# Optimization experiments

Measured on AMD Instinct MI355X. Metric: run time of the kernel, lower is better.

The kernel has to match this reference:

```python
import jax, jax.numpy as jnp
import numpy as np

BS, NQ, NK = 2, 2048, 2048
D_OUT, H, D_K, D_V = 1024, 16, 64, 64


def _xavier(key, shape):
    fan_in, fan_out = shape[1], shape[0]
    lim = float(np.sqrt(6.0 / (fan_in + fan_out)))
    return jax.random.uniform(key, shape, jnp.float32, -lim, lim)


def setup_inputs() -> dict:
    key = jax.random.key(0)
    ks = jax.random.split(key, 9)
    return {
        "queries": jax.random.normal(ks[0], (BS, NQ, D_OUT), jnp.float32),
        "keys": jax.random.normal(ks[1], (BS, NK, D_OUT), jnp.float32),
        "values": jax.random.normal(ks[2], (BS, NK, D_OUT), jnp.float32),
        "mask": jax.random.randint(ks[3], (BS, H, NQ, NK), 0, 2).astype(bool),
        "weights": jax.random.uniform(ks[4], (BS, H, NQ, NK), jnp.float32),
        "Wq": _xavier(ks[5], (H * D_K, D_OUT)),
        "bq": jnp.zeros((H * D_K,), jnp.float32),
        "Wk": _xavier(ks[6], (H * D_K, D_OUT)),
        "bk": jnp.zeros((H * D_K,), jnp.float32),
        "Wv": _xavier(ks[7], (H * D_V, D_OUT)),
        "bv": jnp.zeros((H * D_V,), jnp.float32),
        "Wo": _xavier(ks[8], (D_OUT, H * D_V)),
        "bo": jnp.zeros((D_OUT,), jnp.float32),
    }


def reference(queries, keys, values, mask, weights, Wq, bq, Wk, bk, Wv, bv, Wo, bo):
    bs, nq, _ = queries.shape
    nk = keys.shape[1]
    # projections: (bs, n, h*d) -> (bs, h, n, d)
    q = (queries @ Wq.T + bq).reshape(bs, nq, H, D_K).transpose(0, 2, 1, 3)
    k = (keys @ Wk.T + bk).reshape(bs, nk, H, D_K).transpose(0, 2, 1, 3)
    v = (values @ Wv.T + bv).reshape(bs, nk, H, D_V).transpose(0, 2, 1, 3)
    # scaled dot-product scores: (bs, h, nq, nk)
    att = jnp.einsum("bhqd,bhkd->bhqk", q, k) / jnp.sqrt(jnp.float32(D_K))
    att = att * weights                      # elementwise weight bias
    att = jnp.where(mask, -jnp.inf, att)     # masked_fill(mask, -inf)
    att = jax.nn.softmax(att, axis=-1)
    # dropout is identity at p=0 / eval
    out = jnp.einsum("bhqk,bhkd->bhqd", att, v)  # (bs, h, nq, d_v)
    out = out.transpose(0, 2, 1, 3).reshape(bs, nq, H * D_V)
    return out @ Wo.T + bo
```

## Files before the change

kernel.cpp:

```cpp
#include <hip/hip_runtime.h>
#include <stdint.h>

#define DEV __device__ __forceinline__

typedef __attribute__((__ext_vector_type__(8))) short short8;
typedef __attribute__((__ext_vector_type__(4))) short short4_t;
typedef __attribute__((__ext_vector_type__(4))) float f32x4;
typedef __attribute__((__ext_vector_type__(4))) unsigned short ushort4_t;
typedef __attribute__((__ext_vector_type__(4))) _Float16 half4;

#define MFMA16F16(a, b, c) __builtin_amdgcn_mfma_f32_16x16x16f16((a), (b), (c), 0, 0, 0)

DEV unsigned short f2bf(float f) {
  union { float f; unsigned u; } x; x.f = f;
  unsigned u = x.u;
  unsigned r = (u + 0x7FFFu + ((u >> 16) & 1u)) >> 16;
  return (unsigned short)r;
}

DEV unsigned short f2h(float f) {
  _Float16 h = (_Float16)f;
  unsigned short u;
  __builtin_memcpy(&u, &h, 2);
  return u;
}

DEV void gload_lds16(const void* g, void* l) {
  __builtin_amdgcn_global_load_lds(
      (const __attribute__((address_space(1))) unsigned int*)g,
      (__attribute__((address_space(3))) unsigned int*)l,
      16, 0, 0);
}

DEV short8 ld_g8(const unsigned short* p) { return *(const short8*)p; }
DEV short8 ld_s8(const unsigned short* p) { return *(const short8*)p; }

__global__ void detect_mask_fmt(const unsigned int* __restrict__ mask, int* __restrict__ flag) {
  if (threadIdx.x == 0 && blockIdx.x == 0) {
    int fmt = 1;
    for (int i = 0; i < 256; ++i) {
      unsigned u = mask[i];
      if (u == 0x3F800000u) { fmt = 2; break; }
      if ((u & 0xFFFFFF00u) != 0u) { fmt = 0; break; }
    }
    *flag = fmt;
  }
}

__global__ void cvt_all(const float* __restrict__ q, const float* __restrict__ k,
                        const float* __restrict__ v,
                        const float* __restrict__ wq, const float* __restrict__ wk,
                        const float* __restrict__ wv, const float* __restrict__ wo,
                        unsigned short* __restrict__ Xq, unsigned short* __restrict__ Xk,
                        unsigned short* __restrict__ Xv, unsigned short* __restrict__ Wqb,
                        unsigned short* __restrict__ Wkb, unsigned short* __restrict__ Wvb,
                        unsigned short* __restrict__ Wob) {
  int i = blockIdx.x * 256 + threadIdx.x;
  const float* src; unsigned short* dst; int off;
  if (i < 1048576)      { src = q;  dst = Xq;  off = i; }
  else if (i < 2097152) { src = k;  dst = Xk;  off = i - 1048576; }
  else if (i < 3145728) { src = v;  dst = Xv;  off = i - 2097152; }
  else if (i < 3407872) { src = wq; dst = Wqb; off = i - 3145728; }
  else if (i < 3670016) { src = wk; dst = Wkb; off = i - 3407872; }
  else if (i < 3932160) { src = wv; dst = Wvb; off = i - 3670016; }
  else                  { src = wo; dst = Wob; off = i - 3932160; }
  float4 vv = ((const float4*)src)[off];
  ushort4_t r;
  r.x = f2bf(vv.x); r.y = f2bf(vv.y); r.z = f2bf(vv.z); r.w = f2bf(vv.w);
  ((ushort4_t*)dst)[off] = r;
}

__global__ __launch_bounds__(256, 2) void proj_gemm(
    const unsigned short* __restrict__ Xq, const unsigned short* __restrict__ Xk,
    const unsigned short* __restrict__ Xv,
    const unsigned short* __restrict__ Wqb, const unsigned short* __restrict__ Wkb,
    const unsigned short* __restrict__ Wvb,
    const float* __restrict__ bq, const float* __restrict__ bk, const float* __restrict__ bv,
    unsigned short* __restrict__ QP, unsigned short* __restrict__ KP,
    unsigned short* __restrict__ VT) {
  const int tid = threadIdx.x;
  const int wid = tid >> 6, lane = tid & 63;
  const int l16 = lane & 15, hi = lane >> 4;
  const int m0 = blockIdx.x * 128;
  const int sel = blockIdx.y >> 3;
  const int n0 = (blockIdx.y & 7) * 128;

  const unsigned short* X; const unsigned short* W; const float* bias; unsigned short* out;
  if (sel == 0)      { X = Xq; W = Wqb; bias = bq; out = QP; }
  else if (sel == 1) { X = Xk; W = Wkb; bias = bk; out = KP; }
  else               { X = Xv; W = Wvb; bias = bv; out = VT; }

  __shared__ unsigned short stage[2 * 128 * 32];

  f32x4 acc[4][4] = {};
  const int wm = (wid >> 1) * 64, wn = (wid & 1) * 64;
  const int aoff = (sel == 2) ? 4096 : 0;
  const int boff = 4096 - aoff;

  for (int kt = 0; kt < 1024; kt += 32) {
#pragma unroll
    for (int t = 0; t < 4; ++t) {
      int g = wid * 4 + t;
      int c = g & 7;
      int row = c * 16 + (lane >> 2);
      int ko = (lane & 3) * 8;
      const unsigned short* src = (g < 8)
          ? (X + (size_t)(m0 + row) * 1024 + kt + ko)
          : (W + (size_t)(n0 + row) * 1024 + kt + ko);
      gload_lds16(src, (unsigned short*)((char*)stage + g * 1024));
    }
    __syncthreads();

    short8 af[4], bfr[4];
#pragma unroll
    for (int i = 0; i < 4; ++i)
      af[i] = ld_s8(&stage[aoff + (wm + i * 16 + l16) * 32 + hi * 8]);
#pragma unroll
    for (int j = 0; j < 4; ++j)
      bfr[j] = ld_s8(&stage[boff + (wn + j * 16 + l16) * 32 + hi * 8]);
#pragma unroll
    for (int i = 0; i < 4; ++i)
#pragma unroll
      for (int j = 0; j < 4; ++j)
        acc[i][j] = __builtin_amdgcn_mfma_f32_16x16x32_bf16(af[i], bfr[j], acc[i][j], 0, 0, 0);
    __syncthreads();
  }

  if (sel != 2) {
#pragma unroll
    for (int j = 0; j < 4; ++j) {
      int feat = n0 + wn + j * 16 + l16;
      float bi = bias[feat];
      int h = feat >> 6, d = feat & 63;
#pragma unroll
      for (int i = 0; i < 4; ++i) {
#pragma unroll
        for (int r = 0; r < 4; ++r) {
          int m = m0 + wm + i * 16 + hi * 4 + r;
          int b = m >> 11, n = m & 2047;
          float v = acc[i][j][r] + bi;
          out[(((size_t)(b * 16 + h)) * 2048 + n) * 64 + d] = f2bf(v);
        }
      }
    }
  } else {
#pragma unroll
    for (int j = 0; j < 4; ++j) {
      int tc0 = m0 + wn + j * 16;
      int b = tc0 >> 11, n = tc0 & 2047;
#pragma unroll
      for (int i = 0; i < 4; ++i) {
#pragma unroll
        for (int r = 0; r < 4; ++r) {
          int feat = n0 + wm + i * 16 + hi * 4 + r;
          int h = feat >> 6, d = feat & 63;
          float v = acc[i][j][r] + bias[feat];
          out[((size_t)(b * 16 + h) * 64 + d) * 2048 + n + l16] = f2h(v);
        }
      }
    }
  }
}

__global__ __launch_bounds__(256, 4) void attn_kernel(
    const unsigned short* __restrict__ Q, const unsigned short* __restrict__ K,
    const unsigned short* __restrict__ VT,
    const float* __restrict__ weights,
    const unsigned char* __restrict__ mask8, const unsigned int* __restrict__ mask32,
    const int* __restrict__ mfmt,
    unsigned short* __restrict__ O) {
  const int bid = blockIdx.x;
  const int r8 = bid & 7, g = bid >> 3;
  const int qt = g & 31, bh = r8 + 8 * (g >> 5);
  const int b = bh >> 4, h = bh & 15;
  const int tid = threadIdx.x, wid = tid >> 6, lane = tid & 63;
  const int l16 = lane & 15, hi = lane >> 4;
  const size_t bh_nd = (size_t)bh * 2048 * 64;
  const size_t bh_nn = (size_t)bh * 2048 * 2048;
  const int q0 = qt * 64;
  const int qloc = wid * 16 + l16;
  const int fmt = *mfmt;
  const bool staged_mask = (fmt == 0);

  short8 qf[2];
  qf[0] = ld_g8(Q + bh_nd + (size_t)(q0 + qloc) * 64 + hi * 8);
  qf[1] = ld_g8(Q + bh_nd + (size_t)(q0 + qloc) * 64 + 32 + hi * 8);

  __shared__ float wlds[2][64 * 32];
  __shared__ unsigned short vlds[2][64 * 32];
  __shared__ unsigned char mlds[2][64 * 32];

  const int wr8 = lane >> 3;
  const int wcu = (lane & 7) ^ wr8;
  const size_t woff0 = (size_t)(q0 + wid * 16 + wr8) * 2048 + 4 * wcu;
  const int vr = (lane >> 2) & 15;
  const int vcu = (lane & 3) ^ (vr & 3);
  const size_t voff = (size_t)(wid * 16 + vr) * 2048 + 8 * vcu;
  const int mr = lane >> 1;
  const int mcu = (lane & 1) ^ (mr & 1);
  const size_t moff = (size_t)(q0 + wid * 32 + mr) * 2048 + 16 * mcu;

  const float* wsrc = weights + bh_nn;
  const unsigned short* vsrc = VT + bh_nd;
  const unsigned char* msrc = mask8 + bh_nn;

#define STAGE(NXT, KT)                                                         \
  {                                                                            \
    gload_lds16(wsrc + woff0 + (KT), &wlds[NXT][wid * 512]);                   \
    gload_lds16(wsrc + woff0 + 8 * 2048 + (KT), &wlds[NXT][wid * 512 + 256]);  \
    gload_lds16(vsrc + voff + (KT), &vlds[NXT][wid * 512]);                    \
    if (staged_mask && wid < 2)                                                \
      gload_lds16(msrc + moff + (KT), &mlds[NXT][wid * 1024]);                 \
  }

  f32x4 o[4] = {};
  float mrow = -1e30f, lrow = 0.f;

  STAGE(0, 0)
  __syncthreads();

  for (int t = 0; t < 64; ++t) {
    const int cur = t & 1;
    const int kt0 = t * 32;

    short8 kf00 = ld_g8(K + bh_nd + (size_t)(kt0 + l16) * 64 + hi * 8);
    short8 kf01 = ld_g8(K + bh_nd + (size_t)(kt0 + l16) * 64 + 32 + hi * 8);
    short8 kf10 = ld_g8(K + bh_nd + (size_t)(kt0 + 16 + l16) * 64 + hi * 8);
    short8 kf11 = ld_g8(K + bh_nd + (size_t)(kt0 + 16 + l16) * 64 + 32 + hi * 8);

    if (t < 63) STAGE(cur ^ 1, kt0 + 32)

    f32x4 s0 = {}, s1 = {};
    s0 = __builtin_amdgcn_mfma_f32_16x16x32_bf16(kf00, qf[0], s0, 0, 0, 0);
    s0 = __builtin_amdgcn_mfma_f32_16x16x32_bf16(kf01, qf[1], s0, 0, 0, 0);
    s1 = __builtin_amdgcn_mfma_f32_16x16x32_bf16(kf10, qf[0], s1, 0, 0, 0);
    s1 = __builtin_amdgcn_mfma_f32_16x16x32_bf16(kf11, qf[1], s1, 0, 0, 0);

    f32x4 w0 = *(const f32x4*)&wlds[cur][qloc * 32 + 4 * ((hi + 0) ^ (l16 & 7))];
    f32x4 w1 = *(const f32x4*)&wlds[cur][qloc * 32 + 4 * ((hi + 4) ^ (l16 & 7))];
    unsigned mv0, mv1;
    if (staged_mask) {
      mv0 = *(const unsigned*)&mlds[cur][qloc * 32 + 16 * (0 ^ (l16 & 1)) + 4 * hi];
      mv1 = *(const unsigned*)&mlds[cur][qloc * 32 + 16 * (1 ^ (l16 & 1)) + 4 * hi];
    } else {
      mv0 = mv1 = 0;
      const size_t mb = bh_nn + (size_t)(q0 + qloc) * 2048 + kt0 + 4 * hi;
#pragma unroll
      for (int r = 0; r < 4; ++r) {
        mv0 |= (mask32[mb + r] ? 0xFFu : 0u) << (8 * r);
        mv1 |= (mask32[mb + 16 + r] ? 0xFFu : 0u) << (8 * r);
      }
    }
#pragma unroll
    for (int r = 0; r < 4; ++r) {
      s0[r] = ((mv0 >> (8 * r)) & 0xFF) ? -INFINITY : s0[r] * 0.125f * w0[r];
      s1[r] = ((mv1 >> (8 * r)) & 0xFF) ? -INFINITY : s1[r] * 0.125f * w1[r];
    }

    float tm = fmaxf(fmaxf(fmaxf(s0[0], s0[1]), fmaxf(s0[2], s0[3])),
                     fmaxf(fmaxf(s1[0], s1[1]), fmaxf(s1[2], s1[3])));
    tm = fmaxf(tm, __shfl_xor(tm, 16));
    tm = fmaxf(tm, __shfl_xor(tm, 32));
    float mnew = fmaxf(mrow, tm);
    float sc = __expf(mrow - mnew);
    mrow = mnew;
    lrow *= sc;
#pragma unroll
    for (int d0 = 0; d0 < 4; ++d0) {
      o[d0][0] *= sc; o[d0][1] *= sc; o[d0][2] *= sc; o[d0][3] *= sc;
    }
#pragma unroll
    for (int r = 0; r < 4; ++r) {
      s0[r] = __expf(s0[r] - mrow);
      s1[r] = __expf(s1[r] - mrow);
    }
    float ps = s0[0] + s0[1] + s0[2] + s0[3] + s1[0] + s1[1] + s1[2] + s1[3];
    ps += __shfl_xor(ps, 16);
    ps += __shfl_xor(ps, 32);
    lrow += ps;

    half4 p0, p1;
    p0[0] = (_Float16)s0[0]; p0[1] = (_Float16)s0[1];
    p0[2] = (_Float16)s0[2]; p0[3] = (_Float16)s0[3];
    p1[0] = (_Float16)s1[0]; p1[1] = (_Float16)s1[1];
    p1[2] = (_Float16)s1[2]; p1[3] = (_Float16)s1[3];

#pragma unroll
    for (int d0 = 0; d0 < 4; ++d0) {
      union { short4_t s; half4 h; } v0, v1;
      v0.s = *(const short4_t*)&vlds[cur][(d0 * 16 + l16) * 32 +
              8 * ((2 * 0 + (hi >> 1)) ^ (l16 & 3)) + 4 * (hi & 1)];
      v1.s = *(const short4_t*)&vlds[cur][(d0 * 16 + l16) * 32 +
              8 * ((2 * 1 + (hi >> 1)) ^ (l16 & 3)) + 4 * (hi & 1)];
      o[d0] = MFMA16F16(v0.h, p0, o[d0]);
      o[d0] = MFMA16F16(v1.h, p1, o[d0]);
    }

    __syncthreads();
  }

  float inv = 1.0f / lrow;
  const size_t obase = (size_t)(b * 2048 + q0 + qloc) * 1024 + h * 64;
#pragma unroll
  for (int d0 = 0; d0 < 4; ++d0) {
    ushort4_t pk;
    pk.x = f2bf(o[d0][0] * inv); pk.y = f2bf(o[d0][1] * inv);
    pk.z = f2bf(o[d0][2] * inv); pk.w = f2bf(o[d0][3] * inv);
    *(ushort4_t*)&O[obase + d0 * 16 + 4 * hi] = pk;
  }
#undef STAGE
}

__global__ __launch_bounds__(256, 2) void out_gemm(
    const unsigned short* __restrict__ A, const unsigned short* __restrict__ W,
    const float* __restrict__ bias, float* __restrict__ Cout) {
  const int tid = threadIdx.x;
  const int wid = tid >> 6, lane = tid & 63;
  const int l16 = lane & 15, hi = lane >> 4;
  const int m0 = blockIdx.x * 128;
  const int n0 = blockIdx.y * 128;

  __shared__ unsigned short stage[2 * 128 * 32];
  f32x4 acc[4][4] = {};
  const int wm = (wid >> 1) * 64, wn = (wid & 1) * 64;

  for (int kt = 0; kt < 1024; kt += 32) {
#pragma unroll
    for (int t = 0; t < 4; ++t) {
      int g = wid * 4 + t;
      int c = g & 7;
      int row = c * 16 + (lane >> 2);
      int ko = (lane & 3) * 8;
      const unsigned short* src = (g < 8)
          ? (A + (size_t)(m0 + row) * 1024 + kt + ko)
          : (W + (size_t)(n0 + row) * 1024 + kt + ko);
      gload_lds16(src, (unsigned short*)((char*)stage + g * 1024));
    }
    __syncthreads();

    short8 af[4], bfr[4];
#pragma unroll
    for (int i = 0; i < 4; ++i)
      af[i] = ld_s8(&stage[(wm + i * 16 + l16) * 32 + hi * 8]);
#pragma unroll
    for (int j = 0; j < 4; ++j)
      bfr[j] = ld_s8(&stage[4096 + (wn + j * 16 + l16) * 32 + hi * 8]);
#pragma unroll
    for (int i = 0; i < 4; ++i)
#pragma unroll
      for (int j = 0; j < 4; ++j)
        acc[i][j] = __builtin_amdgcn_mfma_f32_16x16x32_bf16(af[i], bfr[j], acc[i][j], 0, 0, 0);
    __syncthreads();
  }

#pragma unroll
  for (int j = 0; j < 4; ++j) {
    int feat = n0 + wn + j * 16 + l16;
    float bi = bias[feat];
#pragma unroll
    for (int i = 0; i < 4; ++i) {
#pragma unroll
      for (int r = 0; r < 4; ++r) {
        int m = m0 + wm + i * 16 + hi * 4 + r;
        Cout[(size_t)m * 1024 + feat] = acc[i][j][r] + bi;
      }
    }
  }
}

extern "C" void kernel_launch(void* const* d_in, const int* in_sizes, int n_in,
                              void* d_out, int out_size, void* d_ws, size_t ws_size,
                              hipStream_t stream) {
  const float* queries = (const float*)d_in[0];
  const float* keys    = (const float*)d_in[1];
  const float* values  = (const float*)d_in[2];
  const void*  maskp   = d_in[3];
  const float* weights = (const float*)d_in[4];
  const float* Wq = (const float*)d_in[5];
  const float* bq = (const float*)d_in[6];
  const float* Wk = (const float*)d_in[7];
  const float* bk = (const float*)d_in[8];
  const float* Wv = (const float*)d_in[9];
  const float* bv = (const float*)d_in[10];
  const float* Wo = (const float*)d_in[11];
  const float* bo = (const float*)d_in[12];

  unsigned short* ws = (unsigned short*)d_ws;
  unsigned short* Xq  = ws;
  unsigned short* Xk  = ws + 4194304;
  unsigned short* Xv  = ws + 8388608;
  unsigned short* Wqb = ws + 12582912;
  unsigned short* Wkb = ws + 13631488;
  unsigned short* Wvb = ws + 14680064;
  unsigned short* Wob = ws + 15728640;
  unsigned short* QP  = ws + 16777216;
  unsigned short* KP  = ws + 20971520;
  unsigned short* VPT = ws + 25165824;
  unsigned short* OB  = Xq;
  int* mflag = (int*)(ws + 29360128);

  detect_mask_fmt<<<1, 64, 0, stream>>>((const unsigned int*)maskp, mflag);

  cvt_all<<<16384, 256, 0, stream>>>(queries, keys, values, Wq, Wk, Wv, Wo,
                                     Xq, Xk, Xv, Wqb, Wkb, Wvb, Wob);

  proj_gemm<<<dim3(32, 24), 256, 0, stream>>>(Xq, Xk, Xv, Wqb, Wkb, Wvb,
                                              bq, bk, bv, QP, KP, VPT);
  attn_kernel<<<1024, 256, 0, stream>>>(
      QP, KP, VPT, weights,
      (const unsigned char*)maskp, (const unsigned int*)maskp, mflag, OB);
  out_gemm<<<dim3(32, 8), 256, 0, stream>>>(OB, Wob, bo, (float*)d_out);
}
```

Baseline: 387.2 us.

## Pack mask to bits and switch attention to 32x32 MFMA with 128-row tiles

Adds a pre-pass that packs the boolean/int mask into 32-bit bitmasks laid out per key tile, so the attention loop reads one word per row instead of staging bytes. The attention kernel now uses 32x32x16 MFMA for both QK and PV with 128 query rows per block, halving the block count and the redundant K/V reads per query. It also skips the rescale when no lane's running max grows. The cost is an extra kernel pass over the full mask, lower occupancy (launch bounds 2), and a larger weights LDS buffer.

Measured after the change: 359.2 us (median of 2 runs). -7.2%, faster.

```diff
diff --git a/kernel.cpp b/kernel.cpp
--- a/kernel.cpp
+++ b/kernel.cpp
@@ -4,12 +4,11 @@
 #define DEV __device__ __forceinline__
 
 typedef __attribute__((__ext_vector_type__(8))) short short8;
-typedef __attribute__((__ext_vector_type__(4))) short short4_t;
 typedef __attribute__((__ext_vector_type__(4))) float f32x4;
+typedef __attribute__((__ext_vector_type__(16))) float f32x16;
 typedef __attribute__((__ext_vector_type__(4))) unsigned short ushort4_t;
 typedef __attribute__((__ext_vector_type__(4))) _Float16 half4;
-
-#define MFMA16F16(a, b, c) __builtin_amdgcn_mfma_f32_16x16x16f16((a), (b), (c), 0, 0, 0)
+typedef __attribute__((__ext_vector_type__(8))) _Float16 half8;
 
 DEV unsigned short f2bf(float f) {
   union { float f; unsigned u; } x; x.f = f;
@@ -34,6 +33,9 @@
 
 DEV short8 ld_g8(const unsigned short* p) { return *(const short8*)p; }
 DEV short8 ld_s8(const unsigned short* p) { return *(const short8*)p; }
+DEV half4 ld_h4(const unsigned short* p) {
+  half4 r; __builtin_memcpy(&r, p, 8); return r;
+}
 
 __global__ void detect_mask_fmt(const unsigned int* __restrict__ mask, int* __restrict__ flag) {
   if (threadIdx.x == 0 && blockIdx.x == 0) {
@@ -44,6 +46,58 @@
       if ((u & 0xFFFFFF00u) != 0u) { fmt = 0; break; }
     }
     *flag = fmt;
+  }
+}
+
+__global__ void pack_mask(const unsigned char* __restrict__ m8,
+                          const unsigned int* __restrict__ m32,
+                          const int* __restrict__ mfmt,
+                          unsigned int* __restrict__ pm) {
+  __shared__ unsigned int tile[32 * 65];
+  const int bh = blockIdx.x >> 6;
+  const int q0 = (blockIdx.x & 63) * 32;
+  const int fmt = *mfmt;
+  const int tid = threadIdx.x;
+#pragma unroll
+  for (int rnd = 0; rnd < 8; ++rnd) {
+    int w = tid + rnd * 256;
+    int q = w >> 6, t = w & 63;
+    size_t sb = ((size_t)(bh * 2048 + q0 + q)) * 2048 + t * 32;
+    unsigned bits = 0;
+    if (fmt == 0) {
+      uint4 a = *(const uint4*)(m8 + sb);
+      uint4 bq = *(const uint4*)(m8 + sb + 16);
+      unsigned wa0 = a.x, wa1 = a.y, wa2 = a.z, wa3 = a.w;
+      unsigned wb0 = bq.x, wb1 = bq.y, wb2 = bq.z, wb3 = bq.w;
+#pragma unroll
+      for (int e = 0; e < 4; ++e) {
+        bits |= (((wa0 >> (8 * e)) & 0xFFu) ? 1u : 0u) << (0 + e);
+        bits |= (((wa1 >> (8 * e)) & 0xFFu) ? 1u : 0u) << (4 + e);
+        bits |= (((wa2 >> (8 * e)) & 0xFFu) ? 1u : 0u) << (8 + e);
+        bits |= (((wa3 >> (8 * e)) & 0xFFu) ? 1u : 0u) << (12 + e);
+        bits |= (((wb0 >> (8 * e)) & 0xFFu) ? 1u : 0u) << (16 + e);
+        bits |= (((wb1 >> (8 * e)) & 0xFFu) ? 1u : 0u) << (20 + e);
+        bits |= (((wb2 >> (8 * e)) & 0xFFu) ? 1u : 0u) << (24 + e);
+        bits |= (((wb3 >> (8 * e)) & 0xFFu) ? 1u : 0u) << (28 + e);
+      }
+    } else {
+#pragma unroll
+      for (int c = 0; c < 8; ++c) {
+        uint4 v = *(const uint4*)(m32 + sb + c * 4);
+        bits |= (v.x ? 1u : 0u) << (c * 4);
+        bits |= (v.y ? 1u : 0u) << (c * 4 + 1);
+        bits |= (v.z ? 1u : 0u) << (c * 4 + 2);
+        bits |= (v.w ? 1u : 0u) << (c * 4 + 3);
+      }
+    }
+    tile[q * 65 + t] = bits;
+  }
+  __syncthreads();
+#pragma unroll
+  for (int rnd = 0; rnd < 8; ++rnd) {
+    int w = tid + rnd * 256;
+    int t = w >> 5, q = w & 31;
+    pm[((size_t)bh * 64 + t) * 2048 + q0 + q] = tile[q * 65 + t];
   }
 }
 
@@ -162,58 +216,47 @@
   }
 }
 
-__global__ __launch_bounds__(256, 4) void attn_kernel(
+__global__ __launch_bounds__(256, 2) void attn_kernel(
     const unsigned short* __restrict__ Q, const unsigned short* __restrict__ K,
     const unsigned short* __restrict__ VT,
     const float* __restrict__ weights,
-    const unsigned char* __restrict__ mask8, const unsigned int* __restrict__ mask32,
-    const int* __restrict__ mfmt,
+    const unsigned int* __restrict__ pm,
     unsigned short* __restrict__ O) {
   const int bid = blockIdx.x;
-  const int r8 = bid & 7, g = bid >> 3;
-  const int qt = g & 31, bh = r8 + 8 * (g >> 5);
+  const int qt = bid >> 5, bh = bid & 31;
   const int b = bh >> 4, h = bh & 15;
   const int tid = threadIdx.x, wid = tid >> 6, lane = tid & 63;
-  const int l16 = lane & 15, hi = lane >> 4;
+  const int l31 = lane & 31, hh = lane >> 5;
   const size_t bh_nd = (size_t)bh * 2048 * 64;
-  const size_t bh_nn = (size_t)bh * 2048 * 2048;
-  const int q0 = qt * 64;
-  const int qloc = wid * 16 + l16;
-  const int fmt = *mfmt;
-  const bool staged_mask = (fmt == 0);
-
-  short8 qf[2];
-  qf[0] = ld_g8(Q + bh_nd + (size_t)(q0 + qloc) * 64 + hi * 8);
-  qf[1] = ld_g8(Q + bh_nd + (size_t)(q0 + qloc) * 64 + 32 + hi * 8);
-
-  __shared__ float wlds[2][64 * 32];
+  const int q0 = qt * 128;
+  const int qg = q0 + wid * 32 + l31;
+
+  short8 qf0 = ld_g8(Q + bh_nd + (size_t)qg * 64 + 0  + hh * 8);
+  short8 qf1 = ld_g8(Q + bh_nd + (size_t)qg * 64 + 16 + hh * 8);
+  short8 qf2 = ld_g8(Q + bh_nd + (size_t)qg * 64 + 32 + hh * 8);
+  short8 qf3 = ld_g8(Q + bh_nd + (size_t)qg * 64 + 48 + hh * 8);
+
+  __shared__ float wlds[2][128 * 32];
   __shared__ unsigned short vlds[2][64 * 32];
-  __shared__ unsigned char mlds[2][64 * 32];
-
-  const int wr8 = lane >> 3;
-  const int wcu = (lane & 7) ^ wr8;
-  const size_t woff0 = (size_t)(q0 + wid * 16 + wr8) * 2048 + 4 * wcu;
-  const int vr = (lane >> 2) & 15;
-  const int vcu = (lane & 3) ^ (vr & 3);
-  const size_t voff = (size_t)(wid * 16 + vr) * 2048 + 8 * vcu;
-  const int mr = lane >> 1;
-  const int mcu = (lane & 1) ^ (mr & 1);
-  const size_t moff = (size_t)(q0 + wid * 32 + mr) * 2048 + 16 * mcu;
-
-  const float* wsrc = weights + bh_nn;
+
+  const float* wsrc = weights + (size_t)bh * 2048 * 2048;
   const unsigned short* vsrc = VT + bh_nd;
-  const unsigned char* msrc = mask8 + bh_nn;
-
-#define STAGE(NXT, KT)                                                         \
-  {                                                                            \
-    gload_lds16(wsrc + woff0 + (KT), &wlds[NXT][wid * 512]);                   \
-    gload_lds16(wsrc + woff0 + 8 * 2048 + (KT), &wlds[NXT][wid * 512 + 256]);  \
-    gload_lds16(vsrc + voff + (KT), &vlds[NXT][wid * 512]);                    \
-    if (staged_mask && wid < 2)                                                \
-      gload_lds16(msrc + moff + (KT), &mlds[NXT][wid * 1024]);                 \
-  }
-
-  f32x4 o[4] = {};
+  const int wswz = 4 * ((lane & 7) ^ (lane >> 3));
+  const int vswz = 8 * ((lane & 3) ^ ((lane >> 3) & 3));
+  const int wrow_s = q0 + wid * 32 + (lane >> 3);
+  const int vrow_s = wid * 16 + (lane >> 2);
+
+#define STAGE(NXT, KT)                                                        \
+  {                                                                           \
+    _Pragma("unroll")                                                         \
+    for (int i = 0; i < 4; ++i)                                               \
+      gload_lds16(wsrc + (size_t)(wrow_s + i * 8) * 2048 + (KT) + wswz,       \
+                  &wlds[NXT][(wid * 4 + i) * 256]);                           \
+    gload_lds16(vsrc + (size_t)vrow_s * 2048 + (KT) + vswz,                   \
+                &vlds[NXT][wid * 512]);                                       \
+  }
+
+  f32x16 o0 = {}, o1 = {};
   float mrow = -1e30f, lrow = 0.f;
 
   STAGE(0, 0)
@@ -223,90 +266,106 @@
     const int cur = t & 1;
     const int kt0 = t * 32;
 
-    short8 kf00 = ld_g8(K + bh_nd + (size_t)(kt0 + l16) * 64 + hi * 8);
-    short8 kf01 = ld_g8(K + bh_nd + (size_t)(kt0 + l16) * 64 + 32 + hi * 8);
-    short8 kf10 = ld_g8(K + bh_nd + (size_t)(kt0 + 16 + l16) * 64 + hi * 8);
-    short8 kf11 = ld_g8(K + bh_nd + (size_t)(kt0 + 16 + l16) * 64 + 32 + hi * 8);
+    short8 kf0 = ld_g8(K + bh_nd + (size_t)(kt0 + l31) * 64 + 0  + hh * 8);
+    short8 kf1 = ld_g8(K + bh_nd + (size_t)(kt0 + l31) * 64 + 16 + hh * 8);
+    short8 kf2 = ld_g8(K + bh_nd + (size_t)(kt0 + l31) * 64 + 32 + hh * 8);
+    short8 kf3 = ld_g8(K + bh_nd + (size_t)(kt0 + l31) * 64 + 48 + hh * 8);
+    unsigned mw = pm[((size_t)bh * 64 + t) * 2048 + qg];
 
     if (t < 63) STAGE(cur ^ 1, kt0 + 32)
 
-    f32x4 s0 = {}, s1 = {};
-    s0 = __builtin_amdgcn_mfma_f32_16x16x32_bf16(kf00, qf[0], s0, 0, 0, 0);
-    s0 = __builtin_amdgcn_mfma_f32_16x16x32_bf16(kf01, qf[1], s0, 0, 0, 0);
-    s1 = __builtin_amdgcn_mfma_f32_16x16x32_bf16(kf10, qf[0], s1, 0, 0, 0);
-    s1 = __builtin_amdgcn_mfma_f32_16x16x32_bf16(kf11, qf[1], s1, 0, 0, 0);
-
-    f32x4 w0 = *(const f32x4*)&wlds[cur][qloc * 32 + 4 * ((hi + 0) ^ (l16 & 7))];
-    f32x4 w1 = *(const f32x4*)&wlds[cur][qloc * 32 + 4 * ((hi + 4) ^ (l16 & 7))];
-    unsigned mv0, mv1;
-    if (staged_mask) {
-      mv0 = *(const unsigned*)&mlds[cur][qloc * 32 + 16 * (0 ^ (l16 & 1)) + 4 * hi];
-      mv1 = *(const unsigned*)&mlds[cur][qloc * 32 + 16 * (1 ^ (l16 & 1)) + 4 * hi];
-    } else {
-      mv0 = mv1 = 0;
-      const size_t mb = bh_nn + (size_t)(q0 + qloc) * 2048 + kt0 + 4 * hi;
-#pragma unroll
-      for (int r = 0; r < 4; ++r) {
-        mv0 |= (mask32[mb + r] ? 0xFFu : 0u) << (8 * r);
-        mv1 |= (mask32[mb + 16 + r] ? 0xFFu : 0u) << (8 * r);
-      }
-    }
-#pragma unroll
-    for (int r = 0; r < 4; ++r) {
-      s0[r] = ((mv0 >> (8 * r)) & 0xFF) ? -INFINITY : s0[r] * 0.125f * w0[r];
-      s1[r] = ((mv1 >> (8 * r)) & 0xFF) ? -INFINITY : s1[r] * 0.125f * w1[r];
-    }
-
-    float tm = fmaxf(fmaxf(fmaxf(s0[0], s0[1]), fmaxf(s0[2], s0[3])),
-                     fmaxf(fmaxf(s1[0], s1[1]), fmaxf(s1[2], s1[3])));
-    tm = fmaxf(tm, __shfl_xor(tm, 16));
-    tm = fmaxf(tm, __shfl_xor(tm, 32));
-    float mnew = fmaxf(mrow, tm);
-    float sc = __expf(mrow - mnew);
-    mrow = mnew;
-    lrow *= sc;
-#pragma unroll
-    for (int d0 = 0; d0 < 4; ++d0) {
-      o[d0][0] *= sc; o[d0][1] *= sc; o[d0][2] *= sc; o[d0][3] *= sc;
-    }
-#pragma unroll
-    for (int r = 0; r < 4; ++r) {
-      s0[r] = __expf(s0[r] - mrow);
-      s1[r] = __expf(s1[r] - mrow);
-    }
-    float ps = s0[0] + s0[1] + s0[2] + s0[3] + s1[0] + s1[1] + s1[2] + s1[3];
-    ps += __shfl_xor(ps, 16);
-    ps += __shfl_xor(ps, 32);
+    f32x16 s = {};
+    s = __builtin_amdgcn_mfma_f32_32x32x16_bf16(kf0, qf0, s, 0, 0, 0);
+    s = __builtin_amdgcn_mfma_f32_32x32x16_bf16(kf1, qf1, s, 0, 0, 0);
+    s = __builtin_amdgcn_mfma_f32_32x32x16_bf16(kf2, qf2, s, 0, 0, 0);
+    s = __builtin_amdgcn_mfma_f32_32x32x16_bf16(kf3, qf3, s, 0, 0, 0);
+
+    const float* wrow = &wlds[cur][(wid * 32 + l31) * 32];
+    f32x4 wv[4];
+    wv[0] = *(const f32x4*)&wrow[4 * ((hh + 0) ^ (l31 & 7))];
+    wv[1] = *(const f32x4*)&wrow[4 * ((hh + 2) ^ (l31 & 7))];
+    wv[2] = *(const f32x4*)&wrow[4 * ((hh + 4) ^ (l31 & 7))];
+    wv[3] = *(const f32x4*)&wrow[4 * ((hh + 6) ^ (l31 & 7))];
+
+    unsigned mb = mw >> (4 * hh);
+#pragma unroll
+    for (int r = 0; r < 16; ++r) {
+      bool mk = (mb >> ((r & 3) + 8 * (r >> 2))) & 1;
+      s[r] = mk ? -INFINITY : s[r] * 0.125f * wv[r >> 2][r & 3];
+    }
+
+    float tm = s[0];
+#pragma unroll
+    for (int r = 1; r < 16; ++r) tm = fmaxf(tm, s[r]);
+    float tm2 = fmaxf(tm, __shfl_xor(tm, 32));
+    if (__any(tm2 > mrow)) {
+      float mnew = fmaxf(mrow, tm2);
+      float sc = __expf(mrow - mnew);
+      lrow *= sc;
+      o0 *= sc;
+      o1 *= sc;
+      mrow = mnew;
+    }
+    float ps = 0.f;
+#pragma unroll
+    for (int r = 0; r < 16; ++r) {
+      s[r] = __expf(s[r] - mrow);
+      ps += s[r];
+    }
     lrow += ps;
 
-    half4 p0, p1;
-    p0[0] = (_Float16)s0[0]; p0[1] = (_Float16)s0[1];
-    p0[2] = (_Float16)s0[2]; p0[3] = (_Float16)s0[3];
-    p1[0] = (_Float16)s1[0]; p1[1] = (_Float16)s1[1];
-    p1[2] = (_Float16)s1[2]; p1[3] = (_Float16)s1[3];
-
-#pragma unroll
-    for (int d0 = 0; d0 < 4; ++d0) {
-      union { short4_t s; half4 h; } v0, v1;
-      v0.s = *(const short4_t*)&vlds[cur][(d0 * 16 + l16) * 32 +
-              8 * ((2 * 0 + (hi >> 1)) ^ (l16 & 3)) + 4 * (hi & 1)];
-      v1.s = *(const short4_t*)&vlds[cur][(d0 * 16 + l16) * 32 +
-              8 * ((2 * 1 + (hi >> 1)) ^ (l16 & 3)) + 4 * (hi & 1)];
-      o[d0] = MFMA16F16(v0.h, p0, o[d0]);
-      o[d0] = MFMA16F16(v1.h, p1, o[d0]);
+    half8 pa0, pa1;
+#pragma unroll
+    for (int r = 0; r < 8; ++r) {
+      pa0[r] = (_Float16)s[r];
+      pa1[r] = (_Float16)s[8 + r];
+    }
+
+    {
+      const unsigned short* vr = &vlds[cur][l31 * 32];
+      half4 a0 = ld_h4(&vr[4 * ((hh + 0) ^ (l31 & 6))]);
+      half4 a1 = ld_h4(&vr[4 * ((hh + 2) ^ (l31 & 6))]);
+      half8 vf;
+#pragma unroll
+      for (int e = 0; e < 4; ++e) { vf[e] = a0[e]; vf[4 + e] = a1[e]; }
+      o0 = __builtin_amdgcn_mfma_f32_32x32x16_f16(vf, pa0, o0, 0, 0, 0);
+      half4 b0 = ld_h4(&vr[4 * ((hh + 4) ^ (l31 & 6))]);
+      half4 b1 = ld_h4(&vr[4 * ((hh + 6) ^ (l31 & 6))]);
+#pragma unroll
+      for (int e = 0; e < 4; ++e) { vf[e] = b0[e]; vf[4 + e] = b1[e]; }
+      o0 = __builtin_amdgcn_mfma_f32_32x32x16_f16(vf, pa1, o0, 0, 0, 0);
+    }
+    {
+      const unsigned short* vr = &vlds[cur][(32 + l31) * 32];
+      half4 a0 = ld_h4(&vr[4 * ((hh + 0) ^ (l31 & 6))]);
+      half4 a1 = ld_h4(&vr[4 * ((hh + 2) ^ (l31 & 6))]);
+      half8 vf;
+#pragma unroll
+      for (int e = 0; e < 4; ++e) { vf[e] = a0[e]; vf[4 + e] = a1[e]; }
+      o1 = __builtin_amdgcn_mfma_f32_32x32x16_f16(vf, pa0, o1, 0, 0, 0);
+      half4 b0 = ld_h4(&vr[4 * ((hh + 4) ^ (l31 & 6))]);
+      half4 b1 = ld_h4(&vr[4 * ((hh + 6) ^ (l31 & 6))]);
+#pragma unroll
+      for (int e = 0; e < 4; ++e) { vf[e] = b0[e]; vf[4 + e] = b1[e]; }
+      o1 = __builtin_amdgcn_mfma_f32_32x32x16_f16(vf, pa1, o1, 0, 0, 0);
     }
 
     __syncthreads();
   }
 
+  lrow += __shfl_xor(lrow, 32);
   float inv = 1.0f / lrow;
-  const size_t obase = (size_t)(b * 2048 + q0 + qloc) * 1024 + h * 64;
-#pragma unroll
-  for (int d0 = 0; d0 < 4; ++d0) {
+  const size_t ob = (size_t)(b * 2048 + qg) * 1024 + h * 64;
+#pragma unroll
+  for (int j = 0; j < 4; ++j) {
     ushort4_t pk;
-    pk.x = f2bf(o[d0][0] * inv); pk.y = f2bf(o[d0][1] * inv);
-    pk.z = f2bf(o[d0][2] * inv); pk.w = f2bf(o[d0][3] * inv);
-    *(ushort4_t*)&O[obase + d0 * 16 + 4 * hi] = pk;
+    pk.x = f2bf(o0[4 * j + 0] * inv); pk.y = f2bf(o0[4 * j + 1] * inv);
+    pk.z = f2bf(o0[4 * j + 2] * inv); pk.w = f2bf(o0[4 * j + 3] * inv);
+    *(ushort4_t*)&O[ob + 8 * j + 4 * hh] = pk;
+    ushort4_t pk1;
+    pk1.x = f2bf(o1[4 * j + 0] * inv); pk1.y = f2bf(o1[4 * j + 1] * inv);
+    pk1.z = f2bf(o1[4 * j + 2] * inv); pk1.w = f2bf(o1[4 * j + 3] * inv);
+    *(ushort4_t*)&O[ob + 32 + 8 * j + 4 * hh] = pk1;
   }
 #undef STAGE
 }
@@ -397,6 +456,7 @@
   unsigned short* KP  = ws + 20971520;
   unsigned short* VPT = ws + 25165824;
   unsigned short* OB  = Xq;
+  unsigned int* pmb   = (unsigned int*)(ws + 4194304);
   int* mflag = (int*)(ws + 29360128);
 
   detect_mask_fmt<<<1, 64, 0, stream>>>((const unsigned int*)maskp, mflag);
@@ -406,8 +466,11 @@
 
   proj_gemm<<<dim3(32, 24), 256, 0, stream>>>(Xq, Xk, Xv, Wqb, Wkb, Wvb,
                                               bq, bk, bv, QP, KP, VPT);
-  attn_kernel<<<1024, 256, 0, stream>>>(
-      QP, KP, VPT, weights,
-      (const unsigned char*)maskp, (const unsigned int*)maskp, mflag, OB);
+
+  pack_mask<<<2048, 256, 0, stream>>>((const unsigned char*)maskp,
+                                      (const unsigned int*)maskp, mflag, pmb);
+
+  attn_kernel<<<512, 256, 0, stream>>>(QP, KP, VPT, weights, pmb, OB);
+
   out_gemm<<<dim3(32, 8), 256, 0, stream>>>(OB, Wob, bo, (float*)d_out);
 }
```
